# Performance work log

Hardware: AMD Instinct MI355X
Metric: run time of the kernel (lower is better)

The kernel has to match this reference:

```python
import jax, jax.numpy as jnp
import numpy as np

N = 100000
E = 1600000
F_IN = 128
HID = 64
C_OUT = 40


def gcn_conv(x, src, dst, W, b):
    # PyG GCNConv: linear transform, then symmetric-normalized sum aggregation
    n = x.shape[0]
    x = x @ W  # [N, out]
    deg = jax.ops.segment_sum(jnp.ones_like(src, dtype=x.dtype), dst, num_segments=n)
    dinv = jnp.where(deg > 0, jax.lax.rsqrt(deg), 0.0).astype(x.dtype)
    norm = dinv[src] * dinv[dst]  # [E']
    msgs = x[src] * norm[:, None]  # gather + scale
    out = jax.ops.segment_sum(msgs, dst, num_segments=n)  # scatter-add
    return out + b


def setup_inputs() -> dict:
    key = jax.random.key(0)
    k1, k2, k3, k4, k5, k6 = jax.random.split(key, 6)
    x = jax.random.normal(k1, (N, F_IN), dtype=jnp.float32)
    edge_index = jax.random.randint(k2, (2, E), 0, N, dtype=jnp.int64)
    # Glorot-style init for GCNConv linear weights, zero bias (PyG default)
    W1 = jax.random.normal(k3, (F_IN, HID), dtype=jnp.float32) / np.sqrt(F_IN)
    b1 = jnp.zeros((HID,), dtype=jnp.float32)
    W2 = jax.random.normal(k4, (HID, C_OUT), dtype=jnp.float32) / np.sqrt(HID)
    b2 = jnp.zeros((C_OUT,), dtype=jnp.float32)
    return {"x": x, "edge_index": edge_index, "W1": W1, "b1": b1, "W2": W2, "b2": b2}


def reference(x, edge_index, W1, b1, W2, b2):
    n = x.shape[0]
    # add self-loops (PyG GCNConv default add_self_loops=True)
    loops = jnp.arange(n, dtype=edge_index.dtype)
    src = jnp.concatenate([edge_index[0], loops])
    dst = jnp.concatenate([edge_index[1], loops])
    h = gcn_conv(x, src, dst, W1, b1)
    h = jax.nn.relu(h)
    # F.dropout with training=False is identity (eval-mode reference)
    out = gcn_conv(h, src, dst, W2, b2)
    return out
```

## Files before the change

### kernel.cpp

```cpp
#include <hip/hip_runtime.h>

#define F_IN 128
#define HID 64
#define C_OUT 40

#define RB_SHIFT 6
#define RB 64
#define CAP 1408
#define NBMAX 2048
#define FILL_CHUNK 8192
#define FILL_THREADS 512

typedef unsigned short ushort_t;
typedef unsigned int uint_t;
typedef __attribute__((ext_vector_type(8))) short bf16x8;
typedef __attribute__((ext_vector_type(4))) float f32x4;

__device__ __forceinline__ ushort_t f2bf(float f) {
    uint_t u = __float_as_uint(f);
    return (ushort_t)((u + 0x7FFF + ((u >> 16) & 1)) >> 16);
}
__device__ __forceinline__ uint_t cvtpk(float lo, float hi) {
    uint_t r;
    asm("v_cvt_pk_bf16_f32 %0, %1, %2" : "=v"(r) : "v"(lo), "v"(hi));
    return r;
}
__device__ __forceinline__ float bf_lo(uint_t u) { return __uint_as_float(u << 16); }
__device__ __forceinline__ float bf_hi(uint_t u) { return __uint_as_float(u & 0xFFFF0000u); }
__device__ __forceinline__ bf16x8 u4_to_bf(uint4 u) {
    union { uint4 a; bf16x8 b; } cv; cv.a = u; return cv.b;
}

#define ACC8(u) { a[0] += bf_lo(u.x); a[1] += bf_hi(u.x); a[2] += bf_lo(u.y); a[3] += bf_hi(u.y); \
                  a[4] += bf_lo(u.z); a[5] += bf_hi(u.z); a[6] += bf_lo(u.w); a[7] += bf_hi(u.w); }

__global__ __launch_bounds__(FILL_THREADS) void bsort_kernel(
    const int* __restrict__ src, const int* __restrict__ dst, int E,
    int* __restrict__ hist, int* __restrict__ bm, int NB)
{
    __shared__ int lcnt[NBMAX];
    __shared__ int loff[NBMAX];
    __shared__ int wsum[8];
    int t = threadIdx.x;
    for (int i = t; i < NBMAX; i += FILL_THREADS) lcnt[i] = 0;
    __syncthreads();
    int base = blockIdx.x * FILL_CHUNK;
    int nE = min(E - base, FILL_CHUNK);
    #pragma unroll
    for (int k = 0; k < FILL_CHUNK / FILL_THREADS; ++k) {
        int e = k * FILL_THREADS + t;
        if (e < nE) atomicAdd(&lcnt[dst[base + e] >> RB_SHIFT], 1);
    }
    __syncthreads();
    {
        int v[4]; int tsum = 0;
        #pragma unroll
        for (int i = 0; i < 4; ++i) { v[i] = lcnt[t * 4 + i]; tsum += v[i]; }
        int lane = t & 63, wid = t >> 6;
        int incl = tsum;
        #pragma unroll
        for (int off = 1; off < 64; off <<= 1) {
            int u = __shfl_up(incl, off);
            if (lane >= off) incl += u;
        }
        if (lane == 63) wsum[wid] = incl;
        __syncthreads();
        if (t < 8) {
            int w = wsum[t];
            int wincl = w;
            #pragma unroll
            for (int off = 1; off < 8; off <<= 1) {
                int u = __shfl_up(wincl, off);
                if (t >= off) wincl += u;
            }
            wsum[t] = wincl - w;
        }
        __syncthreads();
        int run = wsum[wid] + incl - tsum;
        #pragma unroll
        for (int i = 0; i < 4; ++i) { loff[t * 4 + i] = run; run += v[i]; }
    }
    __syncthreads();
    long long hrow = (long long)blockIdx.x * (NB + 1);
    for (int i = t; i < NB; i += FILL_THREADS) hist[hrow + i] = loff[i];
    if (t == 0) hist[hrow + NB] = nE;
    __syncthreads();
    #pragma unroll
    for (int k = 0; k < FILL_CHUNK / FILL_THREADS; ++k) {
        int e = k * FILL_THREADS + t;
        if (e < nE) {
            int d = dst[base + e], s = src[base + e];
            int b = d >> RB_SHIFT;
            int pos = atomicAdd(&loff[b], 1);
            bm[base + pos] = (s << RB_SHIFT) | (d & (RB - 1));
        }
    }
}

__global__ __launch_bounds__(256) void csr_gather_kernel(
    const int* __restrict__ hist, const int* __restrict__ bm, int K,
    int* __restrict__ csr, int* __restrict__ begp, int* __restrict__ degp,
    float* __restrict__ dinv, int N, int NB)
{
    __shared__ int staging[CAP];
    __shared__ int histo[RB];
    __shared__ int cursor[RB];
    __shared__ int waux[8];
    int t = threadIdx.x;
    int b = blockIdx.x;
    int len = 0, st = 0;
    if (t < K) {
        long long hrow = (long long)t * (NB + 1);
        st = hist[hrow + b];
        len = hist[hrow + b + 1] - st;
    }
    int lane = t & 63, wid = t >> 6;
    int incl = len;
    #pragma unroll
    for (int off = 1; off < 64; off <<= 1) {
        int u = __shfl_up(incl, off);
        if (lane >= off) incl += u;
    }
    if (lane == 63) waux[wid] = incl;
    if (t < RB) histo[t] = 0;
    __syncthreads();
    if (t < 4) {
        int w = waux[t];
        int wincl = w;
        #pragma unroll
        for (int off = 1; off < 4; off <<= 1) {
            int u = __shfl_up(wincl, off);
            if (t >= off) wincl += u;
        }
        waux[t] = wincl - w;
        if (t == 3) waux[4] = wincl;
    }
    __syncthreads();
    int bpos = waux[wid] + incl - len;
    int cnt = waux[4];
    if (cnt > CAP) cnt = CAP;
    if (t < K && len > 0) {
        int gbase = t * FILL_CHUNK + st;
        for (int i = 0; i < len; ++i) {
            int p = bpos + i;
            if (p < CAP) staging[p] = bm[gbase + i];
        }
    }
    __syncthreads();
    for (int i = t; i < cnt; i += 256) atomicAdd(&histo[staging[i] & (RB - 1)], 1);
    __syncthreads();
    if (t < RB) {
        int v = histo[t];
        int nincl = v;
        #pragma unroll
        for (int off = 1; off < 64; off <<= 1) {
            int u = __shfl_up(nincl, off);
            if (t >= off) nincl += u;
        }
        int excl = nincl - v;
        cursor[t] = excl;
        int node = b * RB + t;
        if (node < N) {
            begp[node] = b * CAP + excl;
            degp[node] = v;
            dinv[node] = rsqrtf((float)(v + 1));
        }
    }
    __syncthreads();
    int cbase = b * CAP;
    for (int i = t; i < cnt; i += 256) {
        int e = staging[i];
        int n = e & (RB - 1);
        int r = atomicAdd(&cursor[n], 1);
        csr[cbase + r] = e >> RB_SHIFT;
    }
}

__global__ void wconv_kernel(const float* __restrict__ W1, const float* __restrict__ W2,
                             ushort_t* __restrict__ wb1, ushort_t* __restrict__ wb2)
{
    int tid = blockIdx.x * 256 + threadIdx.x;
    if (tid < 8192) {
        int j = tid & 7, l = (tid >> 3) & 63, ks = (tid >> 9) & 3, ct = tid >> 11;
        int c = ct * 16 + (l & 15);
        int k = ks * 32 + (l >> 4) * 8 + j;
        wb1[tid] = f2bf(W1[k * HID + c]);
    } else if (tid < 8192 + 3072) {
        int s = tid - 8192;
        int j = s & 7, l = (s >> 3) & 63, ks = (s >> 9) & 1, ct = s >> 10;
        int c = ct * 16 + (l & 15);
        int k = ks * 32 + (l >> 4) * 8 + j;
        wb2[s] = (c < C_OUT) ? f2bf(W2[k * C_OUT + c]) : (ushort_t)0;
    }
}

__global__ __launch_bounds__(256) void gemm1_mfma(
    const float* __restrict__ x, const uint_t* __restrict__ Wb,
    const float* __restrict__ dinv, uint_t* __restrict__ y, int N)
{
    __shared__ uint_t ldsW[4096];
    int t = threadIdx.x;
    {
        const uint4* s4 = (const uint4*)Wb;
        uint4* d4 = (uint4*)ldsW;
        for (int i = t; i < 1024; i += 256) d4[i] = s4[i];
    }
    __syncthreads();
    int wid = t >> 6, lane = t & 63;
    int m = lane & 15, kb = lane >> 4;
    int wr = blockIdx.x * 128 + wid * 32;
    int ra0 = min(wr + m, N - 1);
    int ra1 = min(wr + 16 + m, N - 1);
    f32x4 acc[2][4] = {};
    #pragma unroll
    for (int ks = 0; ks < 4; ++ks) {
        const float* p0 = &x[(size_t)ra0 * F_IN + ks * 32 + kb * 8];
        const float* p1 = &x[(size_t)ra1 * F_IN + ks * 32 + kb * 8];
        float4 a0 = *(const float4*)p0, a1 = *(const float4*)(p0 + 4);
        float4 c0 = *(const float4*)p1, c1 = *(const float4*)(p1 + 4);
        uint4 ua = make_uint4(cvtpk(a0.x, a0.y), cvtpk(a0.z, a0.w),
                              cvtpk(a1.x, a1.y), cvtpk(a1.z, a1.w));
        uint4 ub = make_uint4(cvtpk(c0.x, c0.y), cvtpk(c0.z, c0.w),
                              cvtpk(c1.x, c1.y), cvtpk(c1.z, c1.w));
        bf16x8 fa0 = u4_to_bf(ua), fa1 = u4_to_bf(ub);
        #pragma unroll
        for (int ct = 0; ct < 4; ++ct) {
            uint4 wu = *(uint4*)&ldsW[((ct * 4 + ks) * 64 + lane) * 4];
            bf16x8 fb = u4_to_bf(wu);
            acc[0][ct] = __builtin_amdgcn_mfma_f32_16x16x32_bf16(fa0, fb, acc[0][ct], 0, 0, 0);
            acc[1][ct] = __builtin_amdgcn_mfma_f32_16x16x32_bf16(fa1, fb, acc[1][ct], 0, 0, 0);
        }
    }
    int rq = lane >> 4;
    #pragma unroll
    for (int rt = 0; rt < 2; ++rt) {
        float dv[4]; int rows[4];
        #pragma unroll
        for (int j = 0; j < 4; ++j) {
            int r = wr + rt * 16 + rq * 4 + j;
            rows[j] = r;
            dv[j] = dinv[min(r, N - 1)];
        }
        #pragma unroll
        for (int ct = 0; ct < 4; ++ct) {
            #pragma unroll
            for (int j = 0; j < 4; ++j) {
                float v = acc[rt][ct][j] * dv[j];
                float pv = __shfl_xor(v, 1);
                if (!(lane & 1) && rows[j] < N) {
                    y[(size_t)rows[j] * 32 + ct * 8 + (m >> 1)] = cvtpk(v, pv);
                }
            }
        }
    }
}

__global__ __launch_bounds__(256) void agg1_kernel(
    const int* __restrict__ csr, const int* __restrict__ begp, const int* __restrict__ degp,
    const uint_t* __restrict__ y, const float* __restrict__ dinv,
    const float* __restrict__ bias, uint_t* __restrict__ h, int N)
{
    int node = blockIdx.x * 4 + (threadIdx.x >> 6);
    if (node >= N) return;
    int lane = threadIdx.x & 63;
    int o = lane >> 3;
    int c = lane & 7;
    int beg = begp[node];
    int end = beg + degp[node];
    float a[8] = {};
    if (o == 0) {
        uint4 u = *(const uint4*)&y[node * 32 + c * 4];
        ACC8(u);
    }
    int j = beg;
    for (; j + 15 < end; j += 16) {
        int e0 = csr[j + o];
        int e1 = csr[j + 8 + o];
        uint4 u0 = *(const uint4*)&y[e0 * 32 + c * 4];
        uint4 u1 = *(const uint4*)&y[e1 * 32 + c * 4];
        ACC8(u0);
        ACC8(u1);
    }
    for (; j < end; j += 8) {
        if (j + o < end) {
            int e = csr[j + o];
            uint4 u = *(const uint4*)&y[e * 32 + c * 4];
            ACC8(u);
        }
    }
    #pragma unroll
    for (int k = 0; k < 8; ++k) {
        a[k] += __shfl_xor(a[k], 8);
        a[k] += __shfl_xor(a[k], 16);
        a[k] += __shfl_xor(a[k], 32);
    }
    if (o == 0) {
        float di = dinv[node];
        float4 b0 = *(const float4*)&bias[c * 8];
        float4 b1 = *(const float4*)&bias[c * 8 + 4];
        float o0 = fmaxf(a[0] * di + b0.x, 0.f);
        float o1 = fmaxf(a[1] * di + b0.y, 0.f);
        float o2 = fmaxf(a[2] * di + b0.z, 0.f);
        float o3 = fmaxf(a[3] * di + b0.w, 0.f);
        float o4 = fmaxf(a[4] * di + b1.x, 0.f);
        float o5 = fmaxf(a[5] * di + b1.y, 0.f);
        float o6 = fmaxf(a[6] * di + b1.z, 0.f);
        float o7 = fmaxf(a[7] * di + b1.w, 0.f);
        uint4 r = make_uint4(cvtpk(o0, o1), cvtpk(o2, o3), cvtpk(o4, o5), cvtpk(o6, o7));
        *(uint4*)&h[node * 32 + c * 4] = r;
    }
}

__global__ __launch_bounds__(256) void gemm2_mfma(
    const uint_t* __restrict__ h, const uint_t* __restrict__ Wb,
    const float* __restrict__ dinv, uint_t* __restrict__ y, int N)
{
    __shared__ uint_t ldsW[1536];
    int t = threadIdx.x;
    {
        const uint4* s4 = (const uint4*)Wb;
        uint4* d4 = (uint4*)ldsW;
        for (int i = t; i < 384; i += 256) d4[i] = s4[i];
    }
    __syncthreads();
    int wid = t >> 6, lane = t & 63;
    int m = lane & 15, kb = lane >> 4;
    int wr = blockIdx.x * 128 + wid * 32;
    int ra0 = min(wr + m, N - 1);
    int ra1 = min(wr + 16 + m, N - 1);
    f32x4 acc[2][3] = {};
    #pragma unroll
    for (int ks = 0; ks < 2; ++ks) {
        uint4 ua = *(const uint4*)&h[(size_t)ra0 * 32 + ks * 16 + kb * 4];
        uint4 ub = *(const uint4*)&h[(size_t)ra1 * 32 + ks * 16 + kb * 4];
        bf16x8 fa0 = u4_to_bf(ua), fa1 = u4_to_bf(ub);
        #pragma unroll
        for (int ct = 0; ct < 3; ++ct) {
            uint4 wu = *(uint4*)&ldsW[((ct * 2 + ks) * 64 + lane) * 4];
            bf16x8 fb = u4_to_bf(wu);
            acc[0][ct] = __builtin_amdgcn_mfma_f32_16x16x32_bf16(fa0, fb, acc[0][ct], 0, 0, 0);
            acc[1][ct] = __builtin_amdgcn_mfma_f32_16x16x32_bf16(fa1, fb, acc[1][ct], 0, 0, 0);
        }
    }
    int rq = lane >> 4;
    #pragma unroll
    for (int rt = 0; rt < 2; ++rt) {
        float dv[4]; int rows[4];
        #pragma unroll
        for (int j = 0; j < 4; ++j) {
            int r = wr + rt * 16 + rq * 4 + j;
            rows[j] = r;
            dv[j] = dinv[min(r, N - 1)];
        }
        #pragma unroll
        for (int ct = 0; ct < 3; ++ct) {
            #pragma unroll
            for (int j = 0; j < 4; ++j) {
                float v = acc[rt][ct][j] * dv[j];
                float pv = __shfl_xor(v, 1);
                bool colok = (ct < 2) || (m < 8);
                if (!(lane & 1) && colok && rows[j] < N) {
                    y[(size_t)rows[j] * 32 + ct * 8 + (m >> 1)] = cvtpk(v, pv);
                }
            }
        }
    }
}

__global__ __launch_bounds__(256) void agg2_kernel(
    const int* __restrict__ csr, const int* __restrict__ begp, const int* __restrict__ degp,
    const uint_t* __restrict__ y, const float* __restrict__ dinv,
    const float* __restrict__ bias, float* __restrict__ out, int N)
{
    int node = blockIdx.x * 4 + (threadIdx.x >> 6);
    if (node >= N) return;
    int lane = threadIdx.x & 63;
    int o = lane >> 3;
    int c = lane & 7;
    bool act = (c < 5);
    int beg = begp[node];
    int end = beg + degp[node];
    float a[8] = {};
    if (o == 0 && act) {
        uint4 u = *(const uint4*)&y[node * 32 + c * 4];
        ACC8(u);
    }
    int j = beg;
    for (; j + 15 < end; j += 16) {
        if (act) {
            int e0 = csr[j + o];
            int e1 = csr[j + 8 + o];
            uint4 u0 = *(const uint4*)&y[e0 * 32 + c * 4];
            uint4 u1 = *(const uint4*)&y[e1 * 32 + c * 4];
            ACC8(u0);
            ACC8(u1);
        }
    }
    for (; j < end; j += 8) {
        if (j + o < end && act) {
            int e = csr[j + o];
            uint4 u = *(const uint4*)&y[e * 32 + c * 4];
            ACC8(u);
        }
    }
    #pragma unroll
    for (int k = 0; k < 8; ++k) {
        a[k] += __shfl_xor(a[k], 8);
        a[k] += __shfl_xor(a[k], 16);
        a[k] += __shfl_xor(a[k], 32);
    }
    if (o == 0 && act) {
        float di = dinv[node];
        float4 b0 = *(const float4*)&bias[c * 8];
        float4 b1 = *(const float4*)&bias[c * 8 + 4];
        float4 r0, r1;
        r0.x = a[0] * di + b0.x;
        r0.y = a[1] * di + b0.y;
        r0.z = a[2] * di + b0.z;
        r0.w = a[3] * di + b0.w;
        r1.x = a[4] * di + b1.x;
        r1.y = a[5] * di + b1.y;
        r1.z = a[6] * di + b1.z;
        r1.w = a[7] * di + b1.w;
        *(float4*)&out[(size_t)node * C_OUT + c * 8] = r0;
        *(float4*)&out[(size_t)node * C_OUT + c * 8 + 4] = r1;
    }
}

extern "C" void kernel_launch(void* const* d_in, const int* in_sizes, int n_in,
                              void* d_out, int out_size, void* d_ws, size_t ws_size,
                              hipStream_t stream)
{
    const float* x  = (const float*)d_in[0];
    const int*   ei = (const int*)d_in[1];
    const float* W1 = (const float*)d_in[2];
    const float* b1 = (const float*)d_in[3];
    const float* W2 = (const float*)d_in[4];
    const float* b2 = (const float*)d_in[5];
    float* out = (float*)d_out;

    int N = in_sizes[0] / F_IN;
    int E = in_sizes[1] / 2;
    const int* src = ei;
    const int* dst = ei + E;
    int NB = (N + RB - 1) / RB;
    int K = (E + FILL_CHUNK - 1) / FILL_CHUNK;
    int NBLK = (N + 127) / 128;

    char* ws = (char*)d_ws;
    uint_t* y1b    = (uint_t*)ws;  ws += (size_t)N * 32 * 4;
    uint_t* y2b    = (uint_t*)ws;  ws += (size_t)N * 32 * 4;
    uint_t* h1p    = (uint_t*)ws;  ws += (size_t)N * 32 * 4;
    float* dinv    = (float*)ws;   ws += (size_t)N * 4;
    int*   begp    = (int*)ws;     ws += (size_t)N * 4;
    int*   degp    = (int*)ws;     ws += (size_t)N * 4;
    int*   hist    = (int*)ws;     ws += (size_t)K * (NB + 1) * 4;
    int*   bm      = (int*)ws;     ws += (size_t)K * FILL_CHUNK * 4;
    int*   csr     = (int*)ws;     ws += (size_t)NB * CAP * 4;
    ushort_t* wb1  = (ushort_t*)ws; ws += 8192 * 2;
    ushort_t* wb2  = (ushort_t*)ws; ws += 3072 * 2;

    wconv_kernel<<<44, 256, 0, stream>>>(W1, W2, wb1, wb2);

    bsort_kernel<<<K, FILL_THREADS, 0, stream>>>(src, dst, E, hist, bm, NB);
    csr_gather_kernel<<<NB, 256, 0, stream>>>(hist, bm, K, csr, begp, degp, dinv, N, NB);

    gemm1_mfma<<<NBLK, 256, 0, stream>>>(x, (const uint_t*)wb1, dinv, y1b, N);
    agg1_kernel<<<(N + 3) / 4, 256, 0, stream>>>(csr, begp, degp, y1b, dinv, b1, h1p, N);

    gemm2_mfma<<<NBLK, 256, 0, stream>>>(h1p, (const uint_t*)wb2, dinv, y2b, N);
    agg2_kernel<<<(N + 3) / 4, 256, 0, stream>>>(csr, begp, degp, y2b, dinv, b2, out, N);
}
```

Baseline: 154.6 us.

## Persistent aggregation kernels with prefetch of next node's edge indices and packed beg/deg

Both aggregation kernels become grid-stride persistent kernels with a fixed number of blocks. Each wave software-pipelines across its nodes, prefetching the packed begin/degree word two nodes ahead and the first 16 CSR indices one node ahead, so the dependent index-load latency overlaps the current node's feature gathers. Per-node begin offset and degree are packed into one 32-bit word (offset<<11 | degree), which removes one metadata load per node. In exchange, degree is limited to 2047 per node, the load split changes from interleaved halves to per-lane pairs, and a fixed grid may cut parallelism or balance worse across high-degree nodes.

```diff
diff --git a/kernel.cpp b/kernel.cpp
--- a/kernel.cpp
+++ b/kernel.cpp
@@ -10,6 +10,9 @@
 #define NBMAX 2048
 #define FILL_CHUNK 8192
 #define FILL_THREADS 512
+#define AGG_BLOCKS 2048
+
+#define MKBEG(node, b) (((node) >> RB_SHIFT) * CAP + (int)((b) >> 11))
 
 typedef unsigned short ushort_t;
 typedef unsigned int uint_t;
@@ -66,14 +69,14 @@
         if (lane == 63) wsum[wid] = incl;
         __syncthreads();
         if (t < 8) {
-            int w = wsum[t];
-            int wincl = w;
+            int wv = wsum[t];
+            int wincl = wv;
             #pragma unroll
             for (int off = 1; off < 8; off <<= 1) {
                 int u = __shfl_up(wincl, off);
                 if (t >= off) wincl += u;
             }
-            wsum[t] = wincl - w;
+            wsum[t] = wincl - wv;
         }
         __syncthreads();
         int run = wsum[wid] + incl - tsum;
@@ -99,7 +102,7 @@
 
 __global__ __launch_bounds__(256) void csr_gather_kernel(
     const int* __restrict__ hist, const int* __restrict__ bm, int K,
-    int* __restrict__ csr, int* __restrict__ begp, int* __restrict__ degp,
+    int* __restrict__ csr, uint_t* __restrict__ bd,
     float* __restrict__ dinv, int N, int NB)
 {
     __shared__ int staging[CAP];
@@ -161,8 +164,7 @@
         cursor[t] = excl;
         int node = b * RB + t;
         if (node < N) {
-            begp[node] = b * CAP + excl;
-            degp[node] = v;
+            bd[node] = ((uint_t)excl << 11) | (uint_t)v;
             dinv[node] = rsqrtf((float)(v + 1));
         }
     }
@@ -256,58 +258,73 @@
 }
 
 __global__ __launch_bounds__(256) void agg1_kernel(
-    const int* __restrict__ csr, const int* __restrict__ begp, const int* __restrict__ degp,
+    const int* __restrict__ csr, const uint_t* __restrict__ bd,
     const uint_t* __restrict__ y, const float* __restrict__ dinv,
-    const float* __restrict__ bias, uint_t* __restrict__ h, int N)
-{
-    int node = blockIdx.x * 4 + (threadIdx.x >> 6);
-    if (node >= N) return;
+    const float* __restrict__ bias, uint_t* __restrict__ h, int N, int stride)
+{
+    int w = blockIdx.x * 4 + (threadIdx.x >> 6);
+    if (w >= N) return;
     int lane = threadIdx.x & 63;
-    int o = lane >> 3;
-    int c = lane & 7;
-    int beg = begp[node];
-    int end = beg + degp[node];
-    float a[8] = {};
-    if (o == 0) {
-        uint4 u = *(const uint4*)&y[node * 32 + c * 4];
-        ACC8(u);
-    }
-    int j = beg;
-    for (; j + 15 < end; j += 16) {
-        int e0 = csr[j + o];
-        int e1 = csr[j + 8 + o];
-        uint4 u0 = *(const uint4*)&y[e0 * 32 + c * 4];
-        uint4 u1 = *(const uint4*)&y[e1 * 32 + c * 4];
-        ACC8(u0);
-        ACC8(u1);
-    }
-    for (; j < end; j += 8) {
-        if (j + o < end) {
-            int e = csr[j + o];
-            uint4 u = *(const uint4*)&y[e * 32 + c * 4];
+    int o = lane >> 3, c = lane & 7;
+
+    int n1 = w + stride, n2 = w + 2 * stride;
+    uint_t bd0 = bd[w];
+    uint_t bd1 = (n1 < N) ? bd[n1] : 0u;
+    uint2 idx0;
+    {
+        int beg0 = MKBEG(w, bd0), end0 = beg0 + (int)(bd0 & 2047u);
+        int j0 = beg0 + 2 * o;
+        idx0.x = (j0 < end0) ? (uint_t)csr[j0] : 0xFFFFFFFFu;
+        idx0.y = (j0 + 1 < end0) ? (uint_t)csr[j0 + 1] : 0xFFFFFFFFu;
+    }
+
+    for (int node = w; node < N; ) {
+        uint_t bd2 = (n2 < N) ? bd[n2] : 0u;
+        uint2 idx1;
+        {
+            int beg1 = MKBEG(n1, bd1), end1 = beg1 + (int)(bd1 & 2047u);
+            int j0 = beg1 + 2 * o;
+            idx1.x = (j0 < end1) ? (uint_t)csr[j0] : 0xFFFFFFFFu;
+            idx1.y = (j0 + 1 < end1) ? (uint_t)csr[j0 + 1] : 0xFFFFFFFFu;
+        }
+        float a[8] = {};
+        if (o == 0) {
+            uint4 u = *(const uint4*)&y[(size_t)node * 32 + c * 4];
             ACC8(u);
         }
-    }
-    #pragma unroll
-    for (int k = 0; k < 8; ++k) {
-        a[k] += __shfl_xor(a[k], 8);
-        a[k] += __shfl_xor(a[k], 16);
-        a[k] += __shfl_xor(a[k], 32);
-    }
-    if (o == 0) {
-        float di = dinv[node];
-        float4 b0 = *(const float4*)&bias[c * 8];
-        float4 b1 = *(const float4*)&bias[c * 8 + 4];
-        float o0 = fmaxf(a[0] * di + b0.x, 0.f);
-        float o1 = fmaxf(a[1] * di + b0.y, 0.f);
-        float o2 = fmaxf(a[2] * di + b0.z, 0.f);
-        float o3 = fmaxf(a[3] * di + b0.w, 0.f);
-        float o4 = fmaxf(a[4] * di + b1.x, 0.f);
-        float o5 = fmaxf(a[5] * di + b1.y, 0.f);
-        float o6 = fmaxf(a[6] * di + b1.z, 0.f);
-        float o7 = fmaxf(a[7] * di + b1.w, 0.f);
-        uint4 r = make_uint4(cvtpk(o0, o1), cvtpk(o2, o3), cvtpk(o4, o5), cvtpk(o6, o7));
-        *(uint4*)&h[node * 32 + c * 4] = r;
+        if (idx0.x != 0xFFFFFFFFu) { uint4 u = *(const uint4*)&y[(size_t)idx0.x * 32 + c * 4]; ACC8(u); }
+        if (idx0.y != 0xFFFFFFFFu) { uint4 u = *(const uint4*)&y[(size_t)idx0.y * 32 + c * 4]; ACC8(u); }
+        int beg0 = MKBEG(node, bd0), end0 = beg0 + (int)(bd0 & 2047u);
+        for (int j = beg0 + 16; j < end0; j += 16) {
+            int j0 = j + 2 * o;
+            int i0 = (j0 < end0) ? csr[j0] : -1;
+            int i1 = (j0 + 1 < end0) ? csr[j0 + 1] : -1;
+            if (i0 >= 0) { uint4 u = *(const uint4*)&y[(size_t)i0 * 32 + c * 4]; ACC8(u); }
+            if (i1 >= 0) { uint4 u = *(const uint4*)&y[(size_t)i1 * 32 + c * 4]; ACC8(u); }
+        }
+        #pragma unroll
+        for (int k = 0; k < 8; ++k) {
+            a[k] += __shfl_xor(a[k], 8);
+            a[k] += __shfl_xor(a[k], 16);
+            a[k] += __shfl_xor(a[k], 32);
+        }
+        if (o == 0) {
+            float di = dinv[node];
+            float4 b0 = *(const float4*)&bias[c * 8];
+            float4 b1 = *(const float4*)&bias[c * 8 + 4];
+            float o0 = fmaxf(a[0] * di + b0.x, 0.f);
+            float o1 = fmaxf(a[1] * di + b0.y, 0.f);
+            float o2 = fmaxf(a[2] * di + b0.z, 0.f);
+            float o3 = fmaxf(a[3] * di + b0.w, 0.f);
+            float o4 = fmaxf(a[4] * di + b1.x, 0.f);
+            float o5 = fmaxf(a[5] * di + b1.y, 0.f);
+            float o6 = fmaxf(a[6] * di + b1.z, 0.f);
+            float o7 = fmaxf(a[7] * di + b1.w, 0.f);
+            uint4 r = make_uint4(cvtpk(o0, o1), cvtpk(o2, o3), cvtpk(o4, o5), cvtpk(o6, o7));
+            *(uint4*)&h[(size_t)node * 32 + c * 4] = r;
+        }
+        node = n1; n1 = n2; n2 += stride;
+        bd0 = bd1; bd1 = bd2; idx0 = idx1;
     }
 }
 
@@ -368,62 +385,75 @@
 }
 
 __global__ __launch_bounds__(256) void agg2_kernel(
-    const int* __restrict__ csr, const int* __restrict__ begp, const int* __restrict__ degp,
+    const int* __restrict__ csr, const uint_t* __restrict__ bd,
     const uint_t* __restrict__ y, const float* __restrict__ dinv,
-    const float* __restrict__ bias, float* __restrict__ out, int N)
-{
-    int node = blockIdx.x * 4 + (threadIdx.x >> 6);
-    if (node >= N) return;
+    const float* __restrict__ bias, float* __restrict__ out, int N, int stride)
+{
+    int w = blockIdx.x * 4 + (threadIdx.x >> 6);
+    if (w >= N) return;
     int lane = threadIdx.x & 63;
-    int o = lane >> 3;
-    int c = lane & 7;
+    int o = lane >> 3, c = lane & 7;
     bool act = (c < 5);
-    int beg = begp[node];
-    int end = beg + degp[node];
-    float a[8] = {};
-    if (o == 0 && act) {
-        uint4 u = *(const uint4*)&y[node * 32 + c * 4];
-        ACC8(u);
-    }
-    int j = beg;
-    for (; j + 15 < end; j += 16) {
-        if (act) {
-            int e0 = csr[j + o];
-            int e1 = csr[j + 8 + o];
-            uint4 u0 = *(const uint4*)&y[e0 * 32 + c * 4];
-            uint4 u1 = *(const uint4*)&y[e1 * 32 + c * 4];
-            ACC8(u0);
-            ACC8(u1);
-        }
-    }
-    for (; j < end; j += 8) {
-        if (j + o < end && act) {
-            int e = csr[j + o];
-            uint4 u = *(const uint4*)&y[e * 32 + c * 4];
+
+    int n1 = w + stride, n2 = w + 2 * stride;
+    uint_t bd0 = bd[w];
+    uint_t bd1 = (n1 < N) ? bd[n1] : 0u;
+    uint2 idx0;
+    {
+        int beg0 = MKBEG(w, bd0), end0 = beg0 + (int)(bd0 & 2047u);
+        int j0 = beg0 + 2 * o;
+        idx0.x = (j0 < end0) ? (uint_t)csr[j0] : 0xFFFFFFFFu;
+        idx0.y = (j0 + 1 < end0) ? (uint_t)csr[j0 + 1] : 0xFFFFFFFFu;
+    }
+
+    for (int node = w; node < N; ) {
+        uint_t bd2 = (n2 < N) ? bd[n2] : 0u;
+        uint2 idx1;
+        {
+            int beg1 = MKBEG(n1, bd1), end1 = beg1 + (int)(bd1 & 2047u);
+            int j0 = beg1 + 2 * o;
+            idx1.x = (j0 < end1) ? (uint_t)csr[j0] : 0xFFFFFFFFu;
+            idx1.y = (j0 + 1 < end1) ? (uint_t)csr[j0 + 1] : 0xFFFFFFFFu;
+        }
+        float a[8] = {};
+        if (o == 0 && act) {
+            uint4 u = *(const uint4*)&y[(size_t)node * 32 + c * 4];
             ACC8(u);
         }
-    }
-    #pragma unroll
-    for (int k = 0; k < 8; ++k) {
-        a[k] += __shfl_xor(a[k], 8);
-        a[k] += __shfl_xor(a[k], 16);
-        a[k] += __shfl_xor(a[k], 32);
-    }
-    if (o == 0 && act) {
-        float di = dinv[node];
-        float4 b0 = *(const float4*)&bias[c * 8];
-        float4 b1 = *(const float4*)&bias[c * 8 + 4];
-        float4 r0, r1;
-        r0.x = a[0] * di + b0.x;
-        r0.y = a[1] * di + b0.y;
-        r0.z = a[2] * di + b0.z;
-        r0.w = a[3] * di + b0.w;
-        r1.x = a[4] * di + b1.x;
-        r1.y = a[5] * di + b1.y;
-        r1.z = a[6] * di + b1.z;
-        r1.w = a[7] * di + b1.w;
-        *(float4*)&out[(size_t)node * C_OUT + c * 8] = r0;
-        *(float4*)&out[(size_t)node * C_OUT + c * 8 + 4] = r1;
+        if (act && idx0.x != 0xFFFFFFFFu) { uint4 u = *(const uint4*)&y[(size_t)idx0.x * 32 + c * 4]; ACC8(u); }
+        if (act && idx0.y != 0xFFFFFFFFu) { uint4 u = *(const uint4*)&y[(size_t)idx0.y * 32 + c * 4]; ACC8(u); }
+        int beg0 = MKBEG(node, bd0), end0 = beg0 + (int)(bd0 & 2047u);
+        for (int j = beg0 + 16; j < end0; j += 16) {
+            int j0 = j + 2 * o;
+            int i0 = (j0 < end0) ? csr[j0] : -1;
+            int i1 = (j0 + 1 < end0) ? csr[j0 + 1] : -1;
+            if (act && i0 >= 0) { uint4 u = *(const uint4*)&y[(size_t)i0 * 32 + c * 4]; ACC8(u); }
+            if (act && i1 >= 0) { uint4 u = *(const uint4*)&y[(size_t)i1 * 32 + c * 4]; ACC8(u); }
+        }
+        #pragma unroll
+        for (int k = 0; k < 8; ++k) {
+            a[k] += __shfl_xor(a[k], 8);
+            a[k] += __shfl_xor(a[k], 16);
+            a[k] += __shfl_xor(a[k], 32);
+        }
+        if (o == 0 && act) {
+            float di = dinv[node];
+            float4 b0 = *(const float4*)&bias[c * 8];
+            float4 b1 = *(const float4*)&bias[c * 8 + 4];
+            float4 r0, r1;
+            r0.x = a[0] * di + b0.x;
+            r0.y = a[1] * di + b0.y;
+            r0.z = a[2] * di + b0.z;
+            r0.w = a[3] * di + b0.w;
+            r1.x = a[4] * di + b1.x;
+            r1.y = a[5] * di + b1.y;
+            r1.z = a[6] * di + b1.z;
+            r1.w = a[7] * di + b1.w;
+            *(float4*)&out[(size_t)node * C_OUT + c * 8] = r0;
+            *(float4*)&out[(size_t)node * C_OUT + c * 8 + 4] = r1;
+        }
+        node = n1; n1 = n2; n2 += stride;
+        bd0 = bd1; bd1 = bd2; idx0 = idx1;
     }
 }
 
@@ -446,14 +476,14 @@
     int NB = (N + RB - 1) / RB;
     int K = (E + FILL_CHUNK - 1) / FILL_CHUNK;
     int NBLK = (N + 127) / 128;
+    int aggStride = AGG_BLOCKS * 4;
 
     char* ws = (char*)d_ws;
     uint_t* y1b    = (uint_t*)ws;  ws += (size_t)N * 32 * 4;
     uint_t* y2b    = (uint_t*)ws;  ws += (size_t)N * 32 * 4;
     uint_t* h1p    = (uint_t*)ws;  ws += (size_t)N * 32 * 4;
     float* dinv    = (float*)ws;   ws += (size_t)N * 4;
-    int*   begp    = (int*)ws;     ws += (size_t)N * 4;
-    int*   degp    = (int*)ws;     ws += (size_t)N * 4;
+    uint_t* bd     = (uint_t*)ws;  ws += (size_t)N * 4;
     int*   hist    = (int*)ws;     ws += (size_t)K * (NB + 1) * 4;
     int*   bm      = (int*)ws;     ws += (size_t)K * FILL_CHUNK * 4;
     int*   csr     = (int*)ws;     ws += (size_t)NB * CAP * 4;
@@ -463,11 +493,11 @@
     wconv_kernel<<<44, 256, 0, stream>>>(W1, W2, wb1, wb2);
 
     bsort_kernel<<<K, FILL_THREADS, 0, stream>>>(src, dst, E, hist, bm, NB);
-    csr_gather_kernel<<<NB, 256, 0, stream>>>(hist, bm, K, csr, begp, degp, dinv, N, NB);
+    csr_gather_kernel<<<NB, 256, 0, stream>>>(hist, bm, K, csr, bd, dinv, N, NB);
 
     gemm1_mfma<<<NBLK, 256, 0, stream>>>(x, (const uint_t*)wb1, dinv, y1b, N);
-    agg1_kernel<<<(N + 3) / 4, 256, 0, stream>>>(csr, begp, degp, y1b, dinv, b1, h1p, N);
+    agg1_kernel<<<AGG_BLOCKS, 256, 0, stream>>>(csr, bd, y1b, dinv, b1, h1p, N, aggStride);
 
     gemm2_mfma<<<NBLK, 256, 0, stream>>>(h1p, (const uint_t*)wb2, dinv, y2b, N);
-    agg2_kernel<<<(N + 3) / 4, 256, 0, stream>>>(csr, begp, degp, y2b, dinv, b2, out, N);
-}
+    agg2_kernel<<<AGG_BLOCKS, 256, 0, stream>>>(csr, bd, y2b, dinv, b2, out, N, aggStride);
+}
```

Measured after the change: 150.6 us. -2.6%, faster.
